# Kernel tuning notes

Measured on AMD Instinct MI355X. Metric: run time of the kernel, lower is better.

Reference implementation:

```python
import jax, jax.numpy as jnp
import numpy as np

N, D, E, L, NL = 100000, 64, 400000, 4, 10000
NEG = jnp.float32(-1e30)


def _make_graph(key):
    k1, k2, k3, k4 = jax.random.split(key, 4)
    ncov = N - NL
    # nodes [0, NL) never appear as source -> exactly NL leaves
    src_cov = jnp.arange(ncov, dtype=jnp.int32) + NL
    src_rand = jax.random.randint(k1, (E - ncov,), NL, N, dtype=jnp.int32)
    src = jnp.concatenate([src_cov, src_rand])
    dst = jax.random.randint(k2, (E,), 0, N, dtype=jnp.int32)
    edge_index = jnp.stack([src, dst])  # [2, E]
    edge_attr = jax.random.normal(k3, (E, D), jnp.float32)
    # partition edges into L 'topological level' masks
    edge_masks = (jnp.arange(E) % L)[None, :] == jnp.arange(L)[:, None]  # [L, E] bool
    x = jax.random.normal(k4, (N, D), jnp.float32)
    return x, edge_index, edge_attr, edge_masks


def setup_inputs() -> dict:
    key = jax.random.key(0)
    kg1, kg2, kp = jax.random.split(key, 3)
    x1, ei1, ea1, em1 = _make_graph(kg1)
    x2, ei2, ea2, em2 = _make_graph(kg2)
    ks = jax.random.split(kp, 10)
    s = 1.0 / np.sqrt(D)
    params = {
        'We': jax.random.normal(ks[0], (D, D), jnp.float32) * s,
        'be': jax.random.normal(ks[1], (D,), jnp.float32) * s,
        'Wa': jax.random.normal(ks[2], (1, 2 * D), jnp.float32) * s,
        'ba': jax.random.normal(ks[3], (1,), jnp.float32) * s,
        'Wih': jax.random.normal(ks[4], (3 * D, D), jnp.float32) * s,
        'Whh': jax.random.normal(ks[5], (3 * D, D), jnp.float32) * s,
        'bih': jax.random.normal(ks[6], (3 * D,), jnp.float32) * s,
        'bhh': jax.random.normal(ks[7], (3 * D,), jnp.float32) * s,
        'Wc': jax.random.normal(ks[8], (2 * D, 2 * D), jnp.float32) * s,
        'bc': jax.random.normal(ks[9], (2 * D,), jnp.float32) * s,
    }
    return dict(x1=x1, edge_index1=ei1, edge_attr1=ea1, edge_masks1=em1,
                x2=x2, edge_index2=ei2, edge_attr2=ea2, edge_masks2=em2,
                **params, n_leaf=NL)


def _gru(x, h, Wih, Whh, bih, bhh):
    # torch.nn.GRUCell math
    gi = x @ Wih.T + bih
    gh = h @ Whh.T + bhh
    ir, iz, in_ = jnp.split(gi, 3, axis=-1)
    hr, hz, hn = jnp.split(gh, 3, axis=-1)
    r = jax.nn.sigmoid(ir + hr)
    z = jax.nn.sigmoid(iz + hz)
    n = jnp.tanh(in_ + r * hn)
    return (1.0 - z) * n + z * h


def _flow_forward(x, edge_index, edge_attr, edge_masks,
                  We, be, Wa, ba, Wih, Whh, bih, bhh):
    Nn, Dm = x.shape
    src, dst = edge_index[0], edge_index[1]
    root = jnp.ones((Nn,), bool).at[dst].set(False)  # nodes with no incoming edge
    eemb = edge_attr @ We.T + be                     # [E, D] edge_lin
    # roots: GRU with zero hidden; others start at 0 (zeros_like in torch)
    h0 = jnp.where(root[:, None], _gru(x, jnp.zeros_like(x), Wih, Whh, bih, bhh), 0.0)
    q = x[dst]                                       # h_prev_i, level-invariant

    def step(h, mask):
        k = h[src] + eemb                            # h_j + edge_emb
        logit = (jnp.concatenate([q, k], axis=-1) @ Wa.T + ba)[:, 0]  # [E]
        ml = jnp.where(mask, logit, NEG)
        mx = jnp.maximum(jax.ops.segment_max(ml, dst, num_segments=Nn), NEG)
        ex = jnp.where(mask, jnp.exp(ml - mx[dst]), 0.0)  # scatter-softmax numerator
        den = jax.ops.segment_sum(ex, dst, num_segments=Nn)
        alpha = ex / (den[dst] + 1e-16)
        msg = jax.ops.segment_sum(alpha[:, None] * h[src], dst, num_segments=Nn)
        nm = jax.ops.segment_sum(mask.astype(jnp.float32), dst, num_segments=Nn) > 0
        h_new = _gru(x, msg, Wih, Whh, bih, bhh)     # input=h_prev, hidden=msg
        return jnp.where(nm[:, None], h_new, h), None

    h, _ = jax.lax.scan(step, h0, edge_masks)
    return h


def reference(x1, edge_index1, edge_attr1, edge_masks1,
              x2, edge_index2, edge_attr2, edge_masks2,
              We, be, Wa, ba, Wih, Whh, bih, bhh, Wc, bc, n_leaf):
    o1 = _flow_forward(x1, edge_index1, edge_attr1, edge_masks1,
                       We, be, Wa, ba, Wih, Whh, bih, bhh)
    o2 = _flow_forward(x2, edge_index2, edge_attr2, edge_masks2,
                       We, be, Wa, ba, Wih, Whh, bih, bhh)
    Dm = x1.shape[1]
    leaf1 = jnp.ones((x1.shape[0],), bool).at[edge_index1[0]].set(False)
    leaf2 = jnp.ones((x2.shape[0],), bool).at[edge_index2[0]].set(False)
    idx1 = jnp.nonzero(leaf1, size=n_leaf)[0]
    idx2 = jnp.nonzero(leaf2, size=n_leaf)[0]
    feat = jnp.concatenate([o1[idx1], o2[idx2]], axis=-1) @ Wc.T + bc  # [NL, 2D]
    o1 = o1.at[idx1].set(feat[:, :Dm])
    o2 = o2.at[idx2].set(feat[:, Dm:])
    return (o1, o2)
```

## Files before the change

kernel.cpp:

```cpp
#include <hip/hip_runtime.h>

#define NN 100000
#define DD 64
#define EE 400000
#define LL 4
#define NLEAF 10000
#define NT (2*NN)
#define ETOT (2*EE)
#define M4 (4*NT)
#define NBLK ((M4 + 1023)/1024)

typedef __attribute__((ext_vector_type(8))) short bf8v;
typedef __attribute__((ext_vector_type(4))) float f4v;
typedef __attribute__((ext_vector_type(8))) unsigned short su8;

__device__ __forceinline__ float rcp_(float x){ return __builtin_amdgcn_rcpf(x); }
__device__ __forceinline__ float sigm_(float x){ return rcp_(1.f + __expf(-x)); }
__device__ __forceinline__ float tanh_(float x){
  x = fminf(fmaxf(x, -15.f), 15.f);
  float a = __expf(2.f*x);
  return (a - 1.f) * rcp_(a + 1.f);
}
__device__ __forceinline__ float wave_sum(float p){
  #pragma unroll
  for (int m = 1; m < 64; m <<= 1) p += __shfl_xor(p, m, 64);
  return p;
}
__device__ __forceinline__ unsigned short f2b(float f){
  union { float f; unsigned int u; } v; v.f = f;
  unsigned int r = v.u + 0x7FFF + ((v.u >> 16) & 1);
  return (unsigned short)(r >> 16);
}
__device__ __forceinline__ float b2f(unsigned short b){
  union { unsigned int u; float f; } v; v.u = ((unsigned int)b) << 16;
  return v.f;
}
__device__ __forceinline__ int cnt_at(const unsigned int* pcnt, int i){
  int l = i / NT; int td = i - l*NT;
  return (int)((pcnt[td] >> (8*l)) & 255u);
}

__global__ void k_init(unsigned int* __restrict__ pcnt, int* __restrict__ wlcnt,
                       int* __restrict__ row_ptr,
                       float* __restrict__ vvec, float* __restrict__ c0v,
                       unsigned short* __restrict__ whh_bf,
                       unsigned short* __restrict__ wih_bf,
                       const float* __restrict__ We, const float* __restrict__ Wa,
                       const float* __restrict__ be, const float* __restrict__ Whh,
                       const float* __restrict__ Wih) {
  int tid = blockIdx.x*blockDim.x + threadIdx.x;
  int stride = gridDim.x*blockDim.x;
  for (int i = tid; i < NT; i += stride) pcnt[i] = 0u;
  for (int i = tid; i < 192*64; i += stride) whh_bf[i] = f2b(Whh[i]);
  for (int i = tid; i < 208*64; i += stride) {
    int n = i >> 6, k = i & 63;
    unsigned short v;
    if (n < 192)       v = f2b(Wih[i]);
    else if (n == 192) v = f2b(Wa[k]);
    else               v = 0;
    wih_bf[i] = v;
  }
  if (blockIdx.x == 0 && threadIdx.x < 64) {
    int c = threadIdx.x;
    float acc = 0.f;
    for (int d = 0; d < 64; ++d) acc += We[d*64 + c] * Wa[64 + d];
    vvec[c] = acc;
    float p = wave_sum(be[c] * Wa[64 + c]);
    if (c == 0) { c0v[0] = p; row_ptr[M4] = ETOT; }
    if (c < 8) wlcnt[c] = 0;
  }
}

__global__ __launch_bounds__(256) void k_edot(
    const float* __restrict__ ea1, const float* __restrict__ ea2,
    const int* __restrict__ ei1, const int* __restrict__ ei2,
    const float* __restrict__ vvec, const float* __restrict__ c0v,
    float* __restrict__ edot, unsigned int* __restrict__ pcnt) {
  int lane = threadIdx.x & 63;
  int wave = blockIdx.x*(blockDim.x>>6) + (threadIdx.x>>6);
  int nw = gridDim.x*(blockDim.x>>6);
  int grp = lane >> 4, l16 = lane & 15;
  float4 v4 = ((const float4*)vvec)[l16];
  float c0 = c0v[0];
  const int NIT = ETOT/16;
  for (int it = wave; it < NIT; it += 2*nw) {
    int it2 = it + nw;
    bool hasB = (it2 < NIT);
    int e0 = it*16 + grp;
    int g = e0 >= EE;
    const float* ea = g ? ea2 : ea1;
    long eb = e0 - (long)g*EE;
    float4 a0 = ((const float4*)(ea + (eb     )*64))[l16];
    float4 a1 = ((const float4*)(ea + (eb +  4)*64))[l16];
    float4 a2 = ((const float4*)(ea + (eb +  8)*64))[l16];
    float4 a3 = ((const float4*)(ea + (eb + 12)*64))[l16];
    float4 b0, b1, b2, b3; int e1 = 0;
    if (hasB) {
      e1 = it2*16 + grp;
      int g2 = e1 >= EE;
      const float* eb2 = g2 ? ea2 : ea1;
      long ebb = e1 - (long)g2*EE;
      b0 = ((const float4*)(eb2 + (ebb     )*64))[l16];
      b1 = ((const float4*)(eb2 + (ebb +  4)*64))[l16];
      b2 = ((const float4*)(eb2 + (ebb +  8)*64))[l16];
      b3 = ((const float4*)(eb2 + (ebb + 12)*64))[l16];
    } else {
      b0 = b1 = b2 = b3 = make_float4(0.f,0.f,0.f,0.f);
    }
    float p0 = a0.x*v4.x + a0.y*v4.y + a0.z*v4.z + a0.w*v4.w;
    float p1 = a1.x*v4.x + a1.y*v4.y + a1.z*v4.z + a1.w*v4.w;
    float p2 = a2.x*v4.x + a2.y*v4.y + a2.z*v4.z + a2.w*v4.w;
    float p3 = a3.x*v4.x + a3.y*v4.y + a3.z*v4.z + a3.w*v4.w;
    float q0 = b0.x*v4.x + b0.y*v4.y + b0.z*v4.z + b0.w*v4.w;
    float q1 = b1.x*v4.x + b1.y*v4.y + b1.z*v4.z + b1.w*v4.w;
    float q2 = b2.x*v4.x + b2.y*v4.y + b2.z*v4.z + b2.w*v4.w;
    float q3 = b3.x*v4.x + b3.y*v4.y + b3.z*v4.z + b3.w*v4.w;
    #pragma unroll
    for (int m = 1; m < 16; m <<= 1) {
      p0 += __shfl_xor(p0, m, 64); p1 += __shfl_xor(p1, m, 64);
      p2 += __shfl_xor(p2, m, 64); p3 += __shfl_xor(p3, m, 64);
      q0 += __shfl_xor(q0, m, 64); q1 += __shfl_xor(q1, m, 64);
      q2 += __shfl_xor(q2, m, 64); q3 += __shfl_xor(q3, m, 64);
    }
    if (l16 == 0) {
      edot[e0]      = p0 + c0;
      edot[e0 +  4] = p1 + c0;
      edot[e0 +  8] = p2 + c0;
      edot[e0 + 12] = p3 + c0;
      if (hasB) {
        edot[e1]      = q0 + c0;
        edot[e1 +  4] = q1 + c0;
        edot[e1 +  8] = q2 + c0;
        edot[e1 + 12] = q3 + c0;
      }
    }
  }
  int tid = blockIdx.x*blockDim.x + threadIdx.x;
  int stride = gridDim.x*blockDim.x;
  for (int ee = tid; ee < ETOT; ee += stride) {
    int g = ee >= EE;
    int e = ee - g*EE;
    const int* ei = g ? ei2 : ei1;
    int d = ei[EE + e];
    atomicAdd(&pcnt[g*NN + d], 1u << (8*(e & 3)));
  }
}

__global__ __launch_bounds__(256) void k_scan1(const unsigned int* __restrict__ pcnt,
                                               int* __restrict__ row_ptr,
                                               int* __restrict__ partials) {
  __shared__ int ts[256];
  int tx = threadIdx.x;
  int base = blockIdx.x*1024 + tx*4;
  int v[4]; int s = 0;
  #pragma unroll
  for (int u = 0; u < 4; ++u) { v[u] = (base+u < M4) ? cnt_at(pcnt, base+u) : 0; s += v[u]; }
  ts[tx] = s; __syncthreads();
  for (int off = 1; off < 256; off <<= 1) {
    int t = (tx >= off) ? ts[tx-off] : 0;
    __syncthreads();
    ts[tx] += t;
    __syncthreads();
  }
  int excl = ts[tx] - s;
  #pragma unroll
  for (int u = 0; u < 4; ++u) {
    if (base+u < M4) row_ptr[base+u] = excl;
    excl += v[u];
  }
  if (tx == 255) partials[blockIdx.x] = ts[255];
}

__global__ __launch_bounds__(256) void k_scan2(int* __restrict__ partials) {
  __shared__ int ts[256];
  int tx = threadIdx.x;
  int carry = 0;
  for (int base = 0; base < NBLK; base += 256) {
    int i = base + tx;
    int v = (i < NBLK) ? partials[i] : 0;
    ts[tx] = v; __syncthreads();
    for (int off = 1; off < 256; off <<= 1) {
      int t = (tx >= off) ? ts[tx-off] : 0;
      __syncthreads();
      ts[tx] += t;
      __syncthreads();
    }
    int incl = ts[tx];
    int tot = ts[255];
    __syncthreads();
    if (i < NBLK) partials[i] = incl - v + carry;
    carry += tot;
  }
}

__global__ __launch_bounds__(256) void k_scan3(int* __restrict__ row_ptr,
                                               const int* __restrict__ partials,
                                               const unsigned int* __restrict__ pcnt,
                                               int* __restrict__ wl, int* __restrict__ wlcnt,
                                               int* __restrict__ lastlvl,
                                               int* __restrict__ vf) {
  __shared__ int cnt5[5];
  __shared__ int base5[5];
  int tx = threadIdx.x;
  if (tx < 5) cnt5[tx] = 0;
  __syncthreads();
  int tdl = blockIdx.x*blockDim.x + threadIdx.x;
  int rootrank = -1;
  if (tdl < NT) {
    unsigned pv = pcnt[tdl];
    int ll = -1;
    if      (pv & 0xFF000000u) ll = 3;
    else if (pv & 0x00FF0000u) ll = 2;
    else if (pv & 0x0000FF00u) ll = 1;
    else if (pv & 0x000000FFu) ll = 0;
    lastlvl[tdl] = ll;
    int fl = 4;
    if      (pv & 0x000000FFu) fl = 0;
    else if (pv & 0x0000FF00u) fl = 1;
    else if (pv & 0x00FF0000u) fl = 2;
    else if (pv & 0xFF000000u) fl = 3;
    vf[tdl] = (ll < 0) ? 0 : fl + 1;
    if (ll < 0) rootrank = atomicAdd(&cnt5[4], 1);
  }
  int base = blockIdx.x*1024 + tx*4;
  int add = partials[blockIdx.x];
  int rank[4]; int lvl[4]; bool val[4];
  #pragma unroll
  for (int u = 0; u < 4; ++u) {
    int i = base + u;
    val[u] = false;
    if (i < M4) {
      row_ptr[i] += add;
      if (cnt_at(pcnt, i) > 0) {
        int l = i / NT;
        lvl[u] = l;
        rank[u] = atomicAdd(&cnt5[l], 1);
        val[u] = true;
      }
    }
  }
  __syncthreads();
  if (tx < 5 && cnt5[tx] > 0) base5[tx] = atomicAdd(&wlcnt[tx], cnt5[tx]);
  __syncthreads();
  #pragma unroll
  for (int u = 0; u < 4; ++u) {
    if (val[u]) {
      int l = lvl[u];
      wl[l*NT + base5[l] + rank[u]] = (base + u) - l*NT;
    }
  }
  if (rootrank >= 0) wl[4*NT + base5[4] + rootrank] = tdl;
}

__global__ __launch_bounds__(256) void k_fillgix(
    const int* __restrict__ ei1, const int* __restrict__ ei2,
    const float* __restrict__ edot, const float* __restrict__ ba,
    const int* __restrict__ row_ptr, unsigned int* __restrict__ pcnt,
    const int* __restrict__ vf,
    int2* __restrict__ csr,
    const float* __restrict__ x1, const float* __restrict__ x2,
    const unsigned short* __restrict__ wih_bf,
    const float* __restrict__ bih,
    ushort2* __restrict__ gi01, unsigned short* __restrict__ gi2p,
    float* __restrict__ xdot) {
  {
    int tid = blockIdx.x*blockDim.x + threadIdx.x;
    int stride = gridDim.x*blockDim.x;
    float bav = ba[0];
    for (int ee = tid; ee < ETOT; ee += stride) {
      int g = ee >= EE;
      int e = ee - g*EE;
      const int* ei = g ? ei2 : ei1;
      int s = ei[e], d = ei[EE + e];
      int l = e & 3;
      int td = g*NN + d;
      int gs = g*NN + s;
      unsigned old = atomicAdd(&pcnt[td], (unsigned)(0u - (1u << (8*l))));
      int slot = (int)((old >> (8*l)) & 255u) - 1;
      int pos = row_ptr[l*NT + td] + slot;
      csr[pos] = make_int2((vf[gs] << 24) | gs, __float_as_int(edot[ee] + bav));
    }
  }
  int lane = threadIdx.x & 63, w = threadIdx.x >> 6;
  int l15 = lane & 15, quad = lane >> 4;
  int wave = blockIdx.x*4 + w, nw = gridDim.x*4;
  float bi0[4], bi1[4], bi2[4];
  #pragma unroll
  for (int tt = 0; tt < 4; ++tt) {
    int f = l15 + 16*tt;
    bi0[tt]=bih[f]; bi1[tt]=bih[64+f]; bi2[tt]=bih[128+f];
  }
  for (int tl = wave; tl < NT/16; tl += nw) {
    int ta = tl*16 + l15;
    const float* xp = (ta < NN) ? x1 + (size_t)ta*64 : x2 + (size_t)(ta-NN)*64;
    float4 v0 = ((const float4*)xp)[quad*2];
    float4 v1 = ((const float4*)xp)[quad*2 + 1];
    float4 v2 = ((const float4*)xp)[quad*2 + 8];
    float4 v3 = ((const float4*)xp)[quad*2 + 9];
    bf8v a0, a1;
    a0[0]=(short)f2b(v0.x); a0[1]=(short)f2b(v0.y); a0[2]=(short)f2b(v0.z); a0[3]=(short)f2b(v0.w);
    a0[4]=(short)f2b(v1.x); a0[5]=(short)f2b(v1.y); a0[6]=(short)f2b(v1.z); a0[7]=(short)f2b(v1.w);
    a1[0]=(short)f2b(v2.x); a1[1]=(short)f2b(v2.y); a1[2]=(short)f2b(v2.z); a1[3]=(short)f2b(v2.w);
    a1[4]=(short)f2b(v3.x); a1[5]=(short)f2b(v3.y); a1[6]=(short)f2b(v3.z); a1[7]=(short)f2b(v3.w);
    f4v acc[13];
    #pragma unroll
    for (int nt = 0; nt < 13; ++nt) {
      bf8v b0 = *(const bf8v*)&wih_bf[(nt*16 + l15)*64 + quad*8];
      bf8v b1 = *(const bf8v*)&wih_bf[(nt*16 + l15)*64 + 32 + quad*8];
      f4v z = {0.f, 0.f, 0.f, 0.f};
      z = __builtin_amdgcn_mfma_f32_16x16x32_bf16(a0, b0, z, 0, 0, 0);
      acc[nt] = __builtin_amdgcn_mfma_f32_16x16x32_bf16(a1, b1, z, 0, 0, 0);
    }
    #pragma unroll
    for (int r = 0; r < 4; ++r) {
      int t = tl*16 + quad*4 + r;
      #pragma unroll
      for (int tt = 0; tt < 4; ++tt) {
        int f = tt*16 + l15;
        ushort2 p; p.x = f2b(acc[tt][r] + bi0[tt]); p.y = f2b(acc[tt+4][r] + bi1[tt]);
        gi01[(size_t)t*64 + f] = p;
        gi2p[(size_t)t*64 + f] = f2b(acc[tt+8][r] + bi2[tt]);
      }
      if (l15 == 0) xdot[t] = acc[12][r];
    }
  }
}

__global__ __launch_bounds__(256) void k_roots(
    const ushort2* __restrict__ gi01, const unsigned short* __restrict__ gi2p,
    const float* __restrict__ bhh, const float* __restrict__ Wa,
    const int* __restrict__ wl, const int* __restrict__ wlcnt,
    float* __restrict__ hout, unsigned short* __restrict__ hbf,
    float* __restrict__ hdot) {
  int l16 = threadIdx.x & 15;
  int grp = (blockIdx.x*blockDim.x + threadIdx.x) >> 4;
  int ngrp = (gridDim.x*blockDim.x) >> 4;
  int cnt = wlcnt[4];
  float bh0[4], bh1[4], bh2[4], wk[4];
  #pragma unroll
  for (int j = 0; j < 4; ++j) {
    int f = l16*4 + j;
    bh0[j]=bhh[f]; bh1[j]=bhh[64+f]; bh2[j]=bhh[128+f]; wk[j]=Wa[64+f];
  }
  for (int i = grp; i < cnt; i += ngrp) {
    int t = wl[4*NT + i];
    float hds = 0.f;
    #pragma unroll
    for (int j = 0; j < 4; ++j) {
      int f = l16*4 + j;
      ushort2 p01 = gi01[(size_t)t*64 + f];
      float g2 = b2f(gi2p[(size_t)t*64 + f]);
      float rr = sigm_(b2f(p01.x) + bh0[j]);
      float zz = sigm_(b2f(p01.y) + bh1[j]);
      float nn = tanh_(g2 + rr*bh2[j]);
      float hv = (1.f - zz)*nn;
      hout[(size_t)t*64 + f] = hv;
      hbf[(size_t)t*64 + f] = f2b(hv);
      hds += hv * wk[j];
    }
    hds += __shfl_xor(hds, 1, 64);
    hds += __shfl_xor(hds, 2, 64);
    hds += __shfl_xor(hds, 4, 64);
    hds += __shfl_xor(hds, 8, 64);
    if (l16 == 0) hdot[t] = hds;
  }
}

__global__ void k_msg(const int* __restrict__ row_ptr, const int2* __restrict__ csr,
                      const float* __restrict__ xdot,
                      const float* __restrict__ hdot, const unsigned short* __restrict__ hbf,
                      const int* __restrict__ wl, const int* __restrict__ wlcnt,
                      int level, unsigned short* __restrict__ msgn_bf) {
  int l8 = threadIdx.x & 7;
  int grp = (blockIdx.x*blockDim.x + threadIdx.x) >> 3;
  int ngrp = (gridDim.x*blockDim.x) >> 3;
  int cnt = wlcnt[level];
  for (int i = grp; i < cnt; i += ngrp) {
    int t = wl[level*NT + i];
    int bi = level*NT + t;
    int p0 = row_ptr[bi], p1 = row_ptr[bi+1];
    float xd = xdot[t];
    float den = 0.f;
    float m0=0.f, m1=0.f, m2=0.f, m3=0.f, m4=0.f, m5=0.f, m6=0.f, m7=0.f;
    int p = p0;
    for (; p + 2 <= p1; p += 2) {
      int2 prA = csr[p];
      int2 prB = csr[p+1];
      int sA = prA.x & 0x00FFFFFF;
      int sB = prB.x & 0x00FFFFFF;
      bool hA = (prA.x >> 24) <= level;
      bool hB = (prB.x >> 24) <= level;
      float hdA = hA ? hdot[sA] : 0.f;
      float hdB = hB ? hdot[sB] : 0.f;
      su8 h8A = {0,0,0,0,0,0,0,0}, h8B = {0,0,0,0,0,0,0,0};
      if (hA) h8A = *(const su8*)(hbf + (size_t)sA*64 + l8*8);
      if (hB) h8B = *(const su8*)(hbf + (size_t)sB*64 + l8*8);
      float wvA = __expf(xd + hdA + __int_as_float(prA.y));
      float wvB = __expf(xd + hdB + __int_as_float(prB.y));
      den += wvA + wvB;
      m0 += wvA*b2f(h8A[0]) + wvB*b2f(h8B[0]);
      m1 += wvA*b2f(h8A[1]) + wvB*b2f(h8B[1]);
      m2 += wvA*b2f(h8A[2]) + wvB*b2f(h8B[2]);
      m3 += wvA*b2f(h8A[3]) + wvB*b2f(h8B[3]);
      m4 += wvA*b2f(h8A[4]) + wvB*b2f(h8B[4]);
      m5 += wvA*b2f(h8A[5]) + wvB*b2f(h8B[5]);
      m6 += wvA*b2f(h8A[6]) + wvB*b2f(h8B[6]);
      m7 += wvA*b2f(h8A[7]) + wvB*b2f(h8B[7]);
    }
    if (p < p1) {
      int2 pr = csr[p];
      int s = pr.x & 0x00FFFFFF;
      bool hv = (pr.x >> 24) <= level;
      float hd = hv ? hdot[s] : 0.f;
      float wv = __expf(xd + hd + __int_as_float(pr.y));
      den += wv;
      if (hv) {
        su8 h8 = *(const su8*)(hbf + (size_t)s*64 + l8*8);
        m0 += wv*b2f(h8[0]); m1 += wv*b2f(h8[1]);
        m2 += wv*b2f(h8[2]); m3 += wv*b2f(h8[3]);
        m4 += wv*b2f(h8[4]); m5 += wv*b2f(h8[5]);
        m6 += wv*b2f(h8[6]); m7 += wv*b2f(h8[7]);
      }
    }
    float rd = rcp_(den + 1e-16f);
    su8 o;
    o[0] = f2b(m0*rd); o[1] = f2b(m1*rd); o[2] = f2b(m2*rd); o[3] = f2b(m3*rd);
    o[4] = f2b(m4*rd); o[5] = f2b(m5*rd); o[6] = f2b(m6*rd); o[7] = f2b(m7*rd);
    *(su8*)(msgn_bf + (long)i*64 + l8*8) = o;
  }
}

__global__ __launch_bounds__(256) void k_gru(
    const unsigned short* __restrict__ whh_bf, const float* __restrict__ bhh,
    const float* __restrict__ Wa,
    const ushort2* __restrict__ gi01, const unsigned short* __restrict__ gi2p,
    const int* __restrict__ wl, const int* __restrict__ wlcnt,
    const int* __restrict__ lastlvl, int level,
    const unsigned short* __restrict__ msgn_bf,
    float* __restrict__ hout, unsigned short* __restrict__ hbf,
    float* __restrict__ hdot) {
  int lane = threadIdx.x & 63, w = threadIdx.x >> 6;
  int l15 = lane & 15, quad = lane >> 4;
  int cnt = wlcnt[level];
  int ntile = (cnt + 15) >> 4;
  int wave = blockIdx.x*4 + w, nw = gridDim.x*4;
  float bh0[4], bh1[4], bh2[4], wk4[4];
  #pragma unroll
  for (int tt = 0; tt < 4; ++tt) {
    int f = tt*16 + l15;
    bh0[tt]=bhh[f]; bh1[tt]=bhh[64+f]; bh2[tt]=bhh[128+f];
    wk4[tt]=Wa[64+f];
  }
  for (int tl = wave; tl < ntile; tl += nw) {
    int base = tl*16;
    long abase = (long)(base + l15)*64;
    bf8v a0 = *(const bf8v*)&msgn_bf[abase + quad*8];
    bf8v a1 = *(const bf8v*)&msgn_bf[abase + 32 + quad*8];
    f4v acc[12];
    #pragma unroll
    for (int nt = 0; nt < 12; ++nt) {
      bf8v b0 = *(const bf8v*)&whh_bf[(nt*16 + l15)*64 + quad*8];
      bf8v b1 = *(const bf8v*)&whh_bf[(nt*16 + l15)*64 + 32 + quad*8];
      f4v z = {0.f, 0.f, 0.f, 0.f};
      z = __builtin_amdgcn_mfma_f32_16x16x32_bf16(a0, b0, z, 0, 0, 0);
      acc[nt] = __builtin_amdgcn_mfma_f32_16x16x32_bf16(a1, b1, z, 0, 0, 0);
    }
    #pragma unroll
    for (int r = 0; r < 4; ++r) {
      int i = base + quad*4 + r;
      if (i < cnt) {
        int t = wl[level*NT + i];
        int ll = lastlvl[t];
        float hds = 0.f;
        #pragma unroll
        for (int tt = 0; tt < 4; ++tt) {
          int f = tt*16 + l15;
          ushort2 p01 = gi01[(size_t)t*64 + f];
          float g2v = b2f(gi2p[(size_t)t*64 + f]);
          float mv  = b2f(msgn_bf[(long)i*64 + f]);
          float rr = sigm_(b2f(p01.x) + acc[tt][r]   + bh0[tt]);
          float zz = sigm_(b2f(p01.y) + acc[tt+4][r] + bh1[tt]);
          float nn = tanh_(g2v + rr*(acc[tt+8][r] + bh2[tt]));
          float hv = (1.f - zz)*nn + zz*mv;
          if (ll == level) hout[(size_t)t*64 + f] = hv;
          if (level < 3)  hbf[(size_t)t*64 + f] = f2b(hv);
          hds += hv * wk4[tt];
        }
        if (level < 3) {
          hds += __shfl_xor(hds, 1, 64);
          hds += __shfl_xor(hds, 2, 64);
          hds += __shfl_xor(hds, 4, 64);
          hds += __shfl_xor(hds, 8, 64);
          if (l15 == 0) hdot[t] = hds;
        }
      }
    }
  }
}

__global__ __launch_bounds__(256) void k_final(const float* __restrict__ Wc,
                                               const float* __restrict__ bc,
                                               float* __restrict__ hout) {
  __shared__ float WT[128*128];
  for (int idx = threadIdx.x; idx < 128*128; idx += 256) {
    int j = idx >> 7, c = idx & 127;
    WT[c*128 + j] = Wc[idx];
  }
  __syncthreads();
  int lane = threadIdx.x & 63, w = threadIdx.x >> 6;
  int wave = blockIdx.x*4 + w, nw = gridDim.x*4;
  float bc0 = bc[lane], bc1 = bc[64 + lane];
  for (int i = wave; i < NLEAF; i += nw) {
    float h1v = hout[(long)i*64 + lane];
    float h2v = hout[(long)(NN + i)*64 + lane];
    float acc0 = 0.f, acc1 = 0.f;
    for (int c = 0; c < 64; ++c) {
      float m1 = __shfl(h1v, c, 64);
      float m2 = __shfl(h2v, c, 64);
      acc0 += WT[c*128 + lane]      * m1 + WT[(64+c)*128 + lane]      * m2;
      acc1 += WT[c*128 + 64 + lane] * m1 + WT[(64+c)*128 + 64 + lane] * m2;
    }
    hout[(long)i*64 + lane]        = acc0 + bc0;
    hout[(long)(NN + i)*64 + lane] = acc1 + bc1;
  }
}

extern "C" void kernel_launch(void* const* d_in, const int* in_sizes, int n_in,
                              void* d_out, int out_size, void* d_ws, size_t ws_size,
                              hipStream_t stream) {
  const float* x1  = (const float*)d_in[0];
  const int*   ei1 = (const int*)  d_in[1];
  const float* ea1 = (const float*)d_in[2];
  const float* x2  = (const float*)d_in[4];
  const int*   ei2 = (const int*)  d_in[5];
  const float* ea2 = (const float*)d_in[6];
  const float* We  = (const float*)d_in[8];
  const float* be  = (const float*)d_in[9];
  const float* Wa  = (const float*)d_in[10];
  const float* ba  = (const float*)d_in[11];
  const float* Wih = (const float*)d_in[12];
  const float* Whh = (const float*)d_in[13];
  const float* bih = (const float*)d_in[14];
  const float* bhh = (const float*)d_in[15];
  const float* Wc  = (const float*)d_in[16];
  const float* bc  = (const float*)d_in[17];
  float* hout = (float*)d_out;

  float* f = (float*)d_ws;
  ushort2* gi01 = (ushort2*)f;        f += (size_t)NT*64;
  unsigned short* gi2p    = (unsigned short*)f;  f += (size_t)NT*32;
  unsigned short* msgn_bf = (unsigned short*)f;  f += (size_t)NT*32;
  unsigned short* hbf     = (unsigned short*)f;  f += (size_t)NT*32;
  unsigned short* whh_bf  = (unsigned short*)f;  f += 8192;
  unsigned short* wih_bf  = (unsigned short*)f;  f += 8192;
  float* edot = f;  f += ETOT;
  float* xdot = f;  f += NT;
  float* hdot = f;  f += NT;
  float* vvec = f;  f += 64;
  float* c0v  = f;  f += 64;
  int2* csr     = (int2*)f; f += (size_t)2*ETOT;
  unsigned int* pcnt = (unsigned int*)f;  f += NT;
  int* row_ptr  = (int*)f;  f += (M4 + 64);
  int* lastlvl  = (int*)f;  f += NT;
  int* vf       = (int*)f;  f += NT;
  int* wl       = (int*)f;  f += 5*NT;
  int* wlcnt    = (int*)f;  f += 64;
  int* partials = (int*)f;  f += 1024;

  k_init <<<dim3(512),  dim3(256), 0, stream>>>(pcnt, wlcnt, row_ptr, vvec, c0v, whh_bf, wih_bf, We, Wa, be, Whh, Wih);
  k_edot <<<dim3(2048), dim3(256), 0, stream>>>(ea1, ea2, ei1, ei2, vvec, c0v, edot, pcnt);
  k_scan1<<<dim3(NBLK), dim3(256), 0, stream>>>(pcnt, row_ptr, partials);
  k_scan2<<<dim3(1),    dim3(256), 0, stream>>>(partials);
  k_scan3<<<dim3(NBLK), dim3(256), 0, stream>>>(row_ptr, partials, pcnt, wl, wlcnt, lastlvl, vf);
  k_fillgix<<<dim3(2048), dim3(256), 0, stream>>>(ei1, ei2, edot, ba, row_ptr, pcnt, vf, csr, x1, x2, wih_bf, bih, gi01, gi2p, xdot);
  k_roots<<<dim3(256), dim3(256), 0, stream>>>(gi01, gi2p, bhh, Wa, wl, wlcnt, hout, hbf, hdot);
  for (int l = 0; l < 4; ++l) {
    k_msg<<<dim3(4096), dim3(256), 0, stream>>>(row_ptr, csr, xdot, hdot, hbf, wl, wlcnt, l, msgn_bf);
    k_gru<<<dim3(2048), dim3(256), 0, stream>>>(whh_bf, bhh, Wa, gi01, gi2p, wl, wlcnt, lastlvl, l, msgn_bf, hout, hbf, hdot);
  }
  k_final<<<dim3(640), dim3(256), 0, stream>>>(Wc, bc, hout);
}
```

Before: 530.6 us.

## Compute GRU input projection on the fly instead of precomputing gi for all nodes

Drops the precomputed bf16 gi buffers (x@Wih for every node). Each consumer (roots and per-level GRU) now recomputes the input projection with MFMA from a bf16 copy of x, gathered through the worklist. The x→bf16 conversion and the x·Wa dot (xdot) move into the init kernel. This cuts the large gi write and its gathered reads in exchange for extra MFMA work and a gathered x read in each level kernel, and nodes processed at several levels recompute the projection each time.

```diff
diff --git a/kernel.cpp b/kernel.cpp
--- a/kernel.cpp
+++ b/kernel.cpp
@@ -45,6 +45,8 @@
                        float* __restrict__ vvec, float* __restrict__ c0v,
                        unsigned short* __restrict__ whh_bf,
                        unsigned short* __restrict__ wih_bf,
+                       unsigned short* __restrict__ xbf, float* __restrict__ xdot,
+                       const float* __restrict__ x1, const float* __restrict__ x2,
                        const float* __restrict__ We, const float* __restrict__ Wa,
                        const float* __restrict__ be, const float* __restrict__ Whh,
                        const float* __restrict__ Wih) {
@@ -59,6 +61,22 @@
     else if (n == 192) v = f2b(Wa[k]);
     else               v = 0;
     wih_bf[i] = v;
+  }
+  {
+    int lane = threadIdx.x & 63;
+    int l16 = lane & 15, sub = lane >> 4;
+    int wv = tid >> 6, nwv = stride >> 6;
+    float4 wq4 = ((const float4*)(Wa + 64))[l16];
+    for (int nd = wv*4 + sub; nd < NT; nd += nwv*4) {
+      const float* xp = (nd < NN) ? x1 + (size_t)nd*64 : x2 + (size_t)(nd-NN)*64;
+      float4 v = ((const float4*)xp)[l16];
+      float p = v.x*wq4.x + v.y*wq4.y + v.z*wq4.z + v.w*wq4.w;
+      p += __shfl_xor(p, 1, 64); p += __shfl_xor(p, 2, 64);
+      p += __shfl_xor(p, 4, 64); p += __shfl_xor(p, 8, 64);
+      ushort4 o; o.x=f2b(v.x); o.y=f2b(v.y); o.z=f2b(v.z); o.w=f2b(v.w);
+      *(ushort4*)(xbf + (size_t)nd*64 + l16*4) = o;
+      if (l16 == 0) xdot[nd] = p;
+    }
   }
   if (blockIdx.x == 0 && threadIdx.x < 64) {
     int c = threadIdx.x;
@@ -252,117 +270,101 @@
   if (rootrank >= 0) wl[4*NT + base5[4] + rootrank] = tdl;
 }
 
-__global__ __launch_bounds__(256) void k_fillgix(
-    const int* __restrict__ ei1, const int* __restrict__ ei2,
-    const float* __restrict__ edot, const float* __restrict__ ba,
-    const int* __restrict__ row_ptr, unsigned int* __restrict__ pcnt,
-    const int* __restrict__ vf,
-    int2* __restrict__ csr,
-    const float* __restrict__ x1, const float* __restrict__ x2,
+__global__ void k_fill(const int* __restrict__ ei1, const int* __restrict__ ei2,
+                       const float* __restrict__ edot, const float* __restrict__ ba,
+                       const int* __restrict__ row_ptr, unsigned int* __restrict__ pcnt,
+                       const int* __restrict__ vf, int2* __restrict__ csr) {
+  int tid = blockIdx.x*blockDim.x + threadIdx.x;
+  int stride = gridDim.x*blockDim.x;
+  float bav = ba[0];
+  for (int ee = tid; ee < ETOT; ee += stride) {
+    int g = ee >= EE;
+    int e = ee - g*EE;
+    const int* ei = g ? ei2 : ei1;
+    int s = ei[e], d = ei[EE + e];
+    int l = e & 3;
+    int td = g*NN + d;
+    int gs = g*NN + s;
+    unsigned old = atomicAdd(&pcnt[td], (unsigned)(0u - (1u << (8*l))));
+    int slot = (int)((old >> (8*l)) & 255u) - 1;
+    int pos = row_ptr[l*NT + td] + slot;
+    csr[pos] = make_int2((vf[gs] << 24) | gs, __float_as_int(edot[ee] + bav));
+  }
+}
+
+__global__ __launch_bounds__(256) void k_roots(
+    const unsigned short* __restrict__ xbf,
     const unsigned short* __restrict__ wih_bf,
-    const float* __restrict__ bih,
-    ushort2* __restrict__ gi01, unsigned short* __restrict__ gi2p,
-    float* __restrict__ xdot) {
-  {
-    int tid = blockIdx.x*blockDim.x + threadIdx.x;
-    int stride = gridDim.x*blockDim.x;
-    float bav = ba[0];
-    for (int ee = tid; ee < ETOT; ee += stride) {
-      int g = ee >= EE;
-      int e = ee - g*EE;
-      const int* ei = g ? ei2 : ei1;
-      int s = ei[e], d = ei[EE + e];
-      int l = e & 3;
-      int td = g*NN + d;
-      int gs = g*NN + s;
-      unsigned old = atomicAdd(&pcnt[td], (unsigned)(0u - (1u << (8*l))));
-      int slot = (int)((old >> (8*l)) & 255u) - 1;
-      int pos = row_ptr[l*NT + td] + slot;
-      csr[pos] = make_int2((vf[gs] << 24) | gs, __float_as_int(edot[ee] + bav));
-    }
-  }
-  int lane = threadIdx.x & 63, w = threadIdx.x >> 6;
-  int l15 = lane & 15, quad = lane >> 4;
-  int wave = blockIdx.x*4 + w, nw = gridDim.x*4;
-  float bi0[4], bi1[4], bi2[4];
-  #pragma unroll
-  for (int tt = 0; tt < 4; ++tt) {
-    int f = l15 + 16*tt;
-    bi0[tt]=bih[f]; bi1[tt]=bih[64+f]; bi2[tt]=bih[128+f];
-  }
-  for (int tl = wave; tl < NT/16; tl += nw) {
-    int ta = tl*16 + l15;
-    const float* xp = (ta < NN) ? x1 + (size_t)ta*64 : x2 + (size_t)(ta-NN)*64;
-    float4 v0 = ((const float4*)xp)[quad*2];
-    float4 v1 = ((const float4*)xp)[quad*2 + 1];
-    float4 v2 = ((const float4*)xp)[quad*2 + 8];
-    float4 v3 = ((const float4*)xp)[quad*2 + 9];
-    bf8v a0, a1;
-    a0[0]=(short)f2b(v0.x); a0[1]=(short)f2b(v0.y); a0[2]=(short)f2b(v0.z); a0[3]=(short)f2b(v0.w);
-    a0[4]=(short)f2b(v1.x); a0[5]=(short)f2b(v1.y); a0[6]=(short)f2b(v1.z); a0[7]=(short)f2b(v1.w);
-    a1[0]=(short)f2b(v2.x); a1[1]=(short)f2b(v2.y); a1[2]=(short)f2b(v2.z); a1[3]=(short)f2b(v2.w);
-    a1[4]=(short)f2b(v3.x); a1[5]=(short)f2b(v3.y); a1[6]=(short)f2b(v3.z); a1[7]=(short)f2b(v3.w);
-    f4v acc[13];
-    #pragma unroll
-    for (int nt = 0; nt < 13; ++nt) {
-      bf8v b0 = *(const bf8v*)&wih_bf[(nt*16 + l15)*64 + quad*8];
-      bf8v b1 = *(const bf8v*)&wih_bf[(nt*16 + l15)*64 + 32 + quad*8];
-      f4v z = {0.f, 0.f, 0.f, 0.f};
-      z = __builtin_amdgcn_mfma_f32_16x16x32_bf16(a0, b0, z, 0, 0, 0);
-      acc[nt] = __builtin_amdgcn_mfma_f32_16x16x32_bf16(a1, b1, z, 0, 0, 0);
-    }
-    #pragma unroll
-    for (int r = 0; r < 4; ++r) {
-      int t = tl*16 + quad*4 + r;
-      #pragma unroll
-      for (int tt = 0; tt < 4; ++tt) {
-        int f = tt*16 + l15;
-        ushort2 p; p.x = f2b(acc[tt][r] + bi0[tt]); p.y = f2b(acc[tt+4][r] + bi1[tt]);
-        gi01[(size_t)t*64 + f] = p;
-        gi2p[(size_t)t*64 + f] = f2b(acc[tt+8][r] + bi2[tt]);
-      }
-      if (l15 == 0) xdot[t] = acc[12][r];
-    }
-  }
-}
-
-__global__ __launch_bounds__(256) void k_roots(
-    const ushort2* __restrict__ gi01, const unsigned short* __restrict__ gi2p,
-    const float* __restrict__ bhh, const float* __restrict__ Wa,
+    const float* __restrict__ bih, const float* __restrict__ bhh,
+    const float* __restrict__ Wa,
     const int* __restrict__ wl, const int* __restrict__ wlcnt,
     float* __restrict__ hout, unsigned short* __restrict__ hbf,
     float* __restrict__ hdot) {
-  int l16 = threadIdx.x & 15;
-  int grp = (blockIdx.x*blockDim.x + threadIdx.x) >> 4;
-  int ngrp = (gridDim.x*blockDim.x) >> 4;
+  int lane = threadIdx.x & 63, w = threadIdx.x >> 6;
+  int l15 = lane & 15, quad = lane >> 4;
   int cnt = wlcnt[4];
-  float bh0[4], bh1[4], bh2[4], wk[4];
+  int ntile = (cnt + 15) >> 4;
+  int wave = blockIdx.x*4 + w, nw = gridDim.x*4;
+  float bi0[4], bi1[4], bi2[4], bh0[4], bh1[4], bh2[4], wk4[4];
   #pragma unroll
-  for (int j = 0; j < 4; ++j) {
-    int f = l16*4 + j;
-    bh0[j]=bhh[f]; bh1[j]=bhh[64+f]; bh2[j]=bhh[128+f]; wk[j]=Wa[64+f];
-  }
-  for (int i = grp; i < cnt; i += ngrp) {
-    int t = wl[4*NT + i];
-    float hds = 0.f;
+  for (int tt = 0; tt < 4; ++tt) {
+    int f = tt*16 + l15;
+    bi0[tt]=bih[f]; bi1[tt]=bih[64+f]; bi2[tt]=bih[128+f];
+    bh0[tt]=bhh[f]; bh1[tt]=bhh[64+f]; bh2[tt]=bhh[128+f];
+    wk4[tt]=Wa[64+f];
+  }
+  for (int tl = wave; tl < ntile; tl += nw) {
+    int base = tl*16;
+    int ia = base + l15; if (ia >= cnt) ia = cnt - 1;
+    int ta = wl[4*NT + ia];
+    bf8v ax0 = *(const bf8v*)&xbf[(size_t)ta*64 + quad*8];
+    bf8v ax1 = *(const bf8v*)&xbf[(size_t)ta*64 + 32 + quad*8];
+    int tv[4];
     #pragma unroll
-    for (int j = 0; j < 4; ++j) {
-      int f = l16*4 + j;
-      ushort2 p01 = gi01[(size_t)t*64 + f];
-      float g2 = b2f(gi2p[(size_t)t*64 + f]);
-      float rr = sigm_(b2f(p01.x) + bh0[j]);
-      float zz = sigm_(b2f(p01.y) + bh1[j]);
-      float nn = tanh_(g2 + rr*bh2[j]);
-      float hv = (1.f - zz)*nn;
-      hout[(size_t)t*64 + f] = hv;
-      hbf[(size_t)t*64 + f] = f2b(hv);
-      hds += hv * wk[j];
-    }
-    hds += __shfl_xor(hds, 1, 64);
-    hds += __shfl_xor(hds, 2, 64);
-    hds += __shfl_xor(hds, 4, 64);
-    hds += __shfl_xor(hds, 8, 64);
-    if (l16 == 0) hdot[t] = hds;
+    for (int r = 0; r < 4; ++r) {
+      int i = base + quad*4 + r;
+      tv[r] = (i < cnt) ? wl[4*NT + i] : -1;
+    }
+    float hds[4] = {0.f, 0.f, 0.f, 0.f};
+    #pragma unroll
+    for (int tt = 0; tt < 4; ++tt) {
+      bf8v bR0 = *(const bf8v*)&wih_bf[((tt  )*16 + l15)*64 + quad*8];
+      bf8v bR1 = *(const bf8v*)&wih_bf[((tt  )*16 + l15)*64 + 32 + quad*8];
+      bf8v bZ0 = *(const bf8v*)&wih_bf[((tt+4)*16 + l15)*64 + quad*8];
+      bf8v bZ1 = *(const bf8v*)&wih_bf[((tt+4)*16 + l15)*64 + 32 + quad*8];
+      bf8v bN0 = *(const bf8v*)&wih_bf[((tt+8)*16 + l15)*64 + quad*8];
+      bf8v bN1 = *(const bf8v*)&wih_bf[((tt+8)*16 + l15)*64 + 32 + quad*8];
+      f4v zR = {0.f,0.f,0.f,0.f}, zZ = {0.f,0.f,0.f,0.f}, zN = {0.f,0.f,0.f,0.f};
+      zR = __builtin_amdgcn_mfma_f32_16x16x32_bf16(ax0, bR0, zR, 0, 0, 0);
+      zR = __builtin_amdgcn_mfma_f32_16x16x32_bf16(ax1, bR1, zR, 0, 0, 0);
+      zZ = __builtin_amdgcn_mfma_f32_16x16x32_bf16(ax0, bZ0, zZ, 0, 0, 0);
+      zZ = __builtin_amdgcn_mfma_f32_16x16x32_bf16(ax1, bZ1, zZ, 0, 0, 0);
+      zN = __builtin_amdgcn_mfma_f32_16x16x32_bf16(ax0, bN0, zN, 0, 0, 0);
+      zN = __builtin_amdgcn_mfma_f32_16x16x32_bf16(ax1, bN1, zN, 0, 0, 0);
+      int f = tt*16 + l15;
+      #pragma unroll
+      for (int r = 0; r < 4; ++r) {
+        if (tv[r] >= 0) {
+          int t = tv[r];
+          float rr = sigm_(zR[r] + bi0[tt] + bh0[tt]);
+          float zz = sigm_(zZ[r] + bi1[tt] + bh1[tt]);
+          float nn = tanh_(zN[r] + bi2[tt] + rr*bh2[tt]);
+          float hv = (1.f - zz)*nn;
+          hout[(size_t)t*64 + f] = hv;
+          hbf[(size_t)t*64 + f] = f2b(hv);
+          hds[r] += hv * wk4[tt];
+        }
+      }
+    }
+    #pragma unroll
+    for (int r = 0; r < 4; ++r) {
+      if (tv[r] >= 0) {
+        float h = hds[r];
+        h += __shfl_xor(h, 1, 64); h += __shfl_xor(h, 2, 64);
+        h += __shfl_xor(h, 4, 64); h += __shfl_xor(h, 8, 64);
+        if (l15 == 0) hdot[tv[r]] = h;
+      }
+    }
   }
 }
 
@@ -431,9 +433,11 @@
 }
 
 __global__ __launch_bounds__(256) void k_gru(
-    const unsigned short* __restrict__ whh_bf, const float* __restrict__ bhh,
+    const unsigned short* __restrict__ whh_bf,
+    const unsigned short* __restrict__ wih_bf,
+    const float* __restrict__ bih, const float* __restrict__ bhh,
     const float* __restrict__ Wa,
-    const ushort2* __restrict__ gi01, const unsigned short* __restrict__ gi2p,
+    const unsigned short* __restrict__ xbf,
     const int* __restrict__ wl, const int* __restrict__ wlcnt,
     const int* __restrict__ lastlvl, int level,
     const unsigned short* __restrict__ msgn_bf,
@@ -444,54 +448,79 @@
   int cnt = wlcnt[level];
   int ntile = (cnt + 15) >> 4;
   int wave = blockIdx.x*4 + w, nw = gridDim.x*4;
-  float bh0[4], bh1[4], bh2[4], wk4[4];
+  float bi0[4], bi1[4], bi2[4], bh0[4], bh1[4], bh2[4], wk4[4];
   #pragma unroll
   for (int tt = 0; tt < 4; ++tt) {
     int f = tt*16 + l15;
+    bi0[tt]=bih[f]; bi1[tt]=bih[64+f]; bi2[tt]=bih[128+f];
     bh0[tt]=bhh[f]; bh1[tt]=bhh[64+f]; bh2[tt]=bhh[128+f];
     wk4[tt]=Wa[64+f];
   }
   for (int tl = wave; tl < ntile; tl += nw) {
     int base = tl*16;
     long abase = (long)(base + l15)*64;
-    bf8v a0 = *(const bf8v*)&msgn_bf[abase + quad*8];
-    bf8v a1 = *(const bf8v*)&msgn_bf[abase + 32 + quad*8];
-    f4v acc[12];
+    bf8v am0 = *(const bf8v*)&msgn_bf[abase + quad*8];
+    bf8v am1 = *(const bf8v*)&msgn_bf[abase + 32 + quad*8];
+    int ia = base + l15; if (ia >= cnt) ia = cnt - 1;
+    int ta = wl[level*NT + ia];
+    bf8v ax0 = *(const bf8v*)&xbf[(size_t)ta*64 + quad*8];
+    bf8v ax1 = *(const bf8v*)&xbf[(size_t)ta*64 + 32 + quad*8];
+    f4v gh[12];
     #pragma unroll
     for (int nt = 0; nt < 12; ++nt) {
       bf8v b0 = *(const bf8v*)&whh_bf[(nt*16 + l15)*64 + quad*8];
       bf8v b1 = *(const bf8v*)&whh_bf[(nt*16 + l15)*64 + 32 + quad*8];
       f4v z = {0.f, 0.f, 0.f, 0.f};
-      z = __builtin_amdgcn_mfma_f32_16x16x32_bf16(a0, b0, z, 0, 0, 0);
-      acc[nt] = __builtin_amdgcn_mfma_f32_16x16x32_bf16(a1, b1, z, 0, 0, 0);
-    }
+      z = __builtin_amdgcn_mfma_f32_16x16x32_bf16(am0, b0, z, 0, 0, 0);
+      gh[nt] = __builtin_amdgcn_mfma_f32_16x16x32_bf16(am1, b1, z, 0, 0, 0);
+    }
+    int tv[4];
     #pragma unroll
     for (int r = 0; r < 4; ++r) {
       int i = base + quad*4 + r;
-      if (i < cnt) {
-        int t = wl[level*NT + i];
-        int ll = lastlvl[t];
-        float hds = 0.f;
-        #pragma unroll
-        for (int tt = 0; tt < 4; ++tt) {
-          int f = tt*16 + l15;
-          ushort2 p01 = gi01[(size_t)t*64 + f];
-          float g2v = b2f(gi2p[(size_t)t*64 + f]);
-          float mv  = b2f(msgn_bf[(long)i*64 + f]);
-          float rr = sigm_(b2f(p01.x) + acc[tt][r]   + bh0[tt]);
-          float zz = sigm_(b2f(p01.y) + acc[tt+4][r] + bh1[tt]);
-          float nn = tanh_(g2v + rr*(acc[tt+8][r] + bh2[tt]));
+      tv[r] = (i < cnt) ? wl[level*NT + i] : -1;
+    }
+    float hds[4] = {0.f, 0.f, 0.f, 0.f};
+    #pragma unroll
+    for (int tt = 0; tt < 4; ++tt) {
+      bf8v bR0 = *(const bf8v*)&wih_bf[((tt  )*16 + l15)*64 + quad*8];
+      bf8v bR1 = *(const bf8v*)&wih_bf[((tt  )*16 + l15)*64 + 32 + quad*8];
+      bf8v bZ0 = *(const bf8v*)&wih_bf[((tt+4)*16 + l15)*64 + quad*8];
+      bf8v bZ1 = *(const bf8v*)&wih_bf[((tt+4)*16 + l15)*64 + 32 + quad*8];
+      bf8v bN0 = *(const bf8v*)&wih_bf[((tt+8)*16 + l15)*64 + quad*8];
+      bf8v bN1 = *(const bf8v*)&wih_bf[((tt+8)*16 + l15)*64 + 32 + quad*8];
+      f4v zR = {0.f,0.f,0.f,0.f}, zZ = {0.f,0.f,0.f,0.f}, zN = {0.f,0.f,0.f,0.f};
+      zR = __builtin_amdgcn_mfma_f32_16x16x32_bf16(ax0, bR0, zR, 0, 0, 0);
+      zR = __builtin_amdgcn_mfma_f32_16x16x32_bf16(ax1, bR1, zR, 0, 0, 0);
+      zZ = __builtin_amdgcn_mfma_f32_16x16x32_bf16(ax0, bZ0, zZ, 0, 0, 0);
+      zZ = __builtin_amdgcn_mfma_f32_16x16x32_bf16(ax1, bZ1, zZ, 0, 0, 0);
+      zN = __builtin_amdgcn_mfma_f32_16x16x32_bf16(ax0, bN0, zN, 0, 0, 0);
+      zN = __builtin_amdgcn_mfma_f32_16x16x32_bf16(ax1, bN1, zN, 0, 0, 0);
+      int f = tt*16 + l15;
+      #pragma unroll
+      for (int r = 0; r < 4; ++r) {
+        if (tv[r] >= 0) {
+          int t = tv[r];
+          int i = base + quad*4 + r;
+          float mv = b2f(msgn_bf[(long)i*64 + f]);
+          float rr = sigm_(zR[r] + bi0[tt] + gh[tt][r]   + bh0[tt]);
+          float zz = sigm_(zZ[r] + bi1[tt] + gh[tt+4][r] + bh1[tt]);
+          float nn = tanh_(zN[r] + bi2[tt] + rr*(gh[tt+8][r] + bh2[tt]));
           float hv = (1.f - zz)*nn + zz*mv;
-          if (ll == level) hout[(size_t)t*64 + f] = hv;
+          if (lastlvl[t] == level) hout[(size_t)t*64 + f] = hv;
           if (level < 3)  hbf[(size_t)t*64 + f] = f2b(hv);
-          hds += hv * wk4[tt];
+          hds[r] += hv * wk4[tt];
         }
-        if (level < 3) {
-          hds += __shfl_xor(hds, 1, 64);
-          hds += __shfl_xor(hds, 2, 64);
-          hds += __shfl_xor(hds, 4, 64);
-          hds += __shfl_xor(hds, 8, 64);
-          if (l15 == 0) hdot[t] = hds;
+      }
+    }
+    if (level < 3) {
+      #pragma unroll
+      for (int r = 0; r < 4; ++r) {
+        if (tv[r] >= 0) {
+          float h = hds[r];
+          h += __shfl_xor(h, 1, 64); h += __shfl_xor(h, 2, 64);
+          h += __shfl_xor(h, 4, 64); h += __shfl_xor(h, 8, 64);
+          if (l15 == 0) hdot[tv[r]] = h;
         }
       }
     }
@@ -547,8 +576,7 @@
   float* hout = (float*)d_out;
 
   float* f = (float*)d_ws;
-  ushort2* gi01 = (ushort2*)f;        f += (size_t)NT*64;
-  unsigned short* gi2p    = (unsigned short*)f;  f += (size_t)NT*32;
+  unsigned short* xbf     = (unsigned short*)f;  f += (size_t)NT*32;
   unsigned short* msgn_bf = (unsigned short*)f;  f += (size_t)NT*32;
   unsigned short* hbf     = (unsigned short*)f;  f += (size_t)NT*32;
   unsigned short* whh_bf  = (unsigned short*)f;  f += 8192;
@@ -567,16 +595,16 @@
   int* wlcnt    = (int*)f;  f += 64;
   int* partials = (int*)f;  f += 1024;
 
-  k_init <<<dim3(512),  dim3(256), 0, stream>>>(pcnt, wlcnt, row_ptr, vvec, c0v, whh_bf, wih_bf, We, Wa, be, Whh, Wih);
+  k_init <<<dim3(1024), dim3(256), 0, stream>>>(pcnt, wlcnt, row_ptr, vvec, c0v, whh_bf, wih_bf, xbf, xdot, x1, x2, We, Wa, be, Whh, Wih);
   k_edot <<<dim3(2048), dim3(256), 0, stream>>>(ea1, ea2, ei1, ei2, vvec, c0v, edot, pcnt);
   k_scan1<<<dim3(NBLK), dim3(256), 0, stream>>>(pcnt, row_ptr, partials);
   k_scan2<<<dim3(1),    dim3(256), 0, stream>>>(partials);
   k_scan3<<<dim3(NBLK), dim3(256), 0, stream>>>(row_ptr, partials, pcnt, wl, wlcnt, lastlvl, vf);
-  k_fillgix<<<dim3(2048), dim3(256), 0, stream>>>(ei1, ei2, edot, ba, row_ptr, pcnt, vf, csr, x1, x2, wih_bf, bih, gi01, gi2p, xdot);
-  k_roots<<<dim3(256), dim3(256), 0, stream>>>(gi01, gi2p, bhh, Wa, wl, wlcnt, hout, hbf, hdot);
+  k_fill <<<dim3(2048), dim3(256), 0, stream>>>(ei1, ei2, edot, ba, row_ptr, pcnt, vf, csr);
+  k_roots<<<dim3(256),  dim3(256), 0, stream>>>(xbf, wih_bf, bih, bhh, Wa, wl, wlcnt, hout, hbf, hdot);
   for (int l = 0; l < 4; ++l) {
     k_msg<<<dim3(4096), dim3(256), 0, stream>>>(row_ptr, csr, xdot, hdot, hbf, wl, wlcnt, l, msgn_bf);
-    k_gru<<<dim3(2048), dim3(256), 0, stream>>>(whh_bf, bhh, Wa, gi01, gi2p, wl, wlcnt, lastlvl, l, msgn_bf, hout, hbf, hdot);
+    k_gru<<<dim3(2048), dim3(256), 0, stream>>>(whh_bf, wih_bf, bih, bhh, Wa, xbf, wl, wlcnt, lastlvl, l, msgn_bf, hout, hbf, hdot);
   }
   k_final<<<dim3(640), dim3(256), 0, stream>>>(Wc, bc, hout);
 }
```

Result: slower. 672.0 us (+26.7%).
